# Kernel optimization log

Hardware: AMD Instinct MI355X
Metric: run time of the kernel (lower is better)

Reference implementation:

```python
import jax, jax.numpy as jnp
import numpy as np
from functools import partial

D_MODEL = 256
D_STATE = 16
DT_RANK = 16  # ceil(d_model/16)
LN_EPS = 1e-5


def setup_inputs() -> dict:
    key = jax.random.key(0)
    ks = jax.random.split(key, 8)
    B, L, d, N, r = 16, 2048, D_MODEL, D_STATE, DT_RANK
    x = jax.random.normal(ks[0], (B, L, d), dtype=jnp.float32)
    # LayerNorm params
    ln_w = jnp.ones((d,), jnp.float32)
    ln_b = jnp.zeros((d,), jnp.float32)
    # S6 params
    x_proj_w = jax.random.normal(ks[1], (d, r + 2 * N), jnp.float32) / np.sqrt(d)
    dt_proj_w = jax.random.normal(ks[2], (r, d), jnp.float32) / np.sqrt(r)
    dt_proj_b = jax.random.uniform(ks[3], (d,), jnp.float32, -4.0, -2.0)  # softplus -> small dt
    A_log = jnp.log(jnp.tile(jnp.arange(1, N + 1, dtype=jnp.float32), (d, 1)))  # (d, N)
    D_skip = jnp.ones((d,), jnp.float32)
    # GLU params
    glu_w = jax.random.normal(ks[4], (d, 2 * d), jnp.float32) / np.sqrt(d)
    glu_b = jnp.zeros((2 * d,), jnp.float32)
    return {"x": x, "ln_w": ln_w, "ln_b": ln_b, "x_proj_w": x_proj_w,
            "dt_proj_w": dt_proj_w, "dt_proj_b": dt_proj_b, "A_log": A_log,
            "D_skip": D_skip, "glu_w": glu_w, "glu_b": glu_b}


def _layernorm(x, w, b):
    mu = jnp.mean(x, -1, keepdims=True)
    var = jnp.mean(jnp.square(x - mu), -1, keepdims=True)
    return (x - mu) * jax.lax.rsqrt(var + LN_EPS) * w + b


def _s6(x, x_proj_w, dt_proj_w, dt_proj_b, A_log, D_skip):
    # x: (B, L, d) selective scan (S6)
    Bsz, L, d = x.shape
    N = A_log.shape[1]
    A = -jnp.exp(A_log)                       # (d, N)
    dbl = x @ x_proj_w                        # (B, L, r+2N)
    dt, Bm, Cm = jnp.split(dbl, [DT_RANK, DT_RANK + N], axis=-1)
    delta = jax.nn.softplus(dt @ dt_proj_w + dt_proj_b)  # (B, L, d)

    def step(h, inp):
        d_t, b_t, c_t, x_t = inp              # (B,d),(B,N),(B,N),(B,d)
        dA = jnp.exp(d_t[..., None] * A)      # (B, d, N)
        h = dA * h + (d_t * x_t)[..., None] * b_t[:, None, :]
        y = jnp.einsum('bdn,bn->bd', h, c_t)
        return h, y

    h0 = jnp.zeros((Bsz, d, N), x.dtype)
    xs = (jnp.swapaxes(delta, 0, 1), jnp.swapaxes(Bm, 0, 1),
          jnp.swapaxes(Cm, 0, 1), jnp.swapaxes(x, 0, 1))
    _, ys = jax.lax.scan(step, h0, xs)        # ys: (L, B, d)
    return jnp.swapaxes(ys, 0, 1) + x * D_skip


def _glu(x, w, b):
    d = x.shape[-1]
    out = x @ w + b
    return out[..., :d] * jax.nn.sigmoid(out[..., d:])


@jax.jit
def reference(x, ln_w, ln_b, x_proj_w, dt_proj_w, dt_proj_b, A_log, D_skip, glu_w, glu_b):
    skip = x
    h = _layernorm(x, ln_w, ln_b)
    h = _s6(h, x_proj_w, dt_proj_w, dt_proj_b, A_log, D_skip)
    h = jax.nn.gelu(h, approximate=False)     # dropout = identity (eval)
    h = _glu(h, glu_w, glu_b)
    return h + skip
```

## Files before the change

### kernel.cpp

```cpp
#include <hip/hip_runtime.h>
#include <hip/hip_bf16.h>

#define BB 16
#define LL 2048
#define DD 256
#define NN 16
#define RR 16
#define CHF 32
#define LCF 64
#define CHB 64
#define LCB 32

static __device__ __forceinline__ float bf2f(unsigned short u) {
    return __uint_as_float(((unsigned)u) << 16);
}
static __device__ __forceinline__ unsigned short f2bf(float f) {
    unsigned u = __float_as_uint(f);
    u += 0x7FFFu + ((u >> 16) & 1u);
    return (unsigned short)(u >> 16);
}

typedef __attribute__((ext_vector_type(8))) short bf16x8;
typedef __attribute__((ext_vector_type(4))) short bf16x4;
typedef __attribute__((ext_vector_type(4))) float f32x4;

static __device__ __forceinline__ void pow_tree(float E, float* e) {
    e[0] = E;
    e[1] = E * E;
    e[2] = e[1] * E;
    e[3] = e[1] * e[1];
    e[4] = e[3] * e[0];  e[5] = e[3] * e[1];  e[6] = e[3] * e[2];  e[7] = e[3] * e[3];
    e[8] = e[7] * e[0];  e[9] = e[7] * e[1];  e[10] = e[7] * e[2]; e[11] = e[7] * e[3];
    e[12] = e[7] * e[4]; e[13] = e[7] * e[5]; e[14] = e[7] * e[6]; e[15] = e[7] * e[7];
}

static __device__ __forceinline__ void gridBarrier(unsigned* bar, unsigned nblk) {
    __threadfence();
    __syncthreads();
    if (threadIdx.x == 0) {
        unsigned* cnt = bar;
        unsigned* gen = bar + 32;
        const unsigned gsnap = atomicAdd(gen, 0u);
        const unsigned arrived = atomicAdd(cnt, 1u) + 1u;
        if (arrived == nblk) {
            atomicExch(cnt, 0u);
            __threadfence();
            atomicAdd(gen, 1u);
        } else {
            while (atomicAdd(gen, 0u) == gsnap)
                __builtin_amdgcn_s_sleep(2);
        }
    }
    __syncthreads();
    __threadfence();
}

__global__ __launch_bounds__(256) void k_prep(
    const float* __restrict__ xw, const float* __restrict__ gw,
    unsigned short* __restrict__ Wxt, unsigned short* __restrict__ Wt)
{
    __shared__ unsigned short s[32][33];
    const int bid = blockIdx.x;
    const int t = threadIdx.x;
    if (bid < 16) {
        const int idx = bid * 256 + t;
        const int n  = idx >> 6;
        const int k0 = (idx & 63) * 4;
        #pragma unroll
        for (int i = 0; i < 4; ++i) {
            float v = (n < 48) ? xw[(size_t)(k0 + i) * 48 + n] : 0.f;
            Wxt[(size_t)n * DD + k0 + i] = f2bf(v);
        }
    } else {
        const int bb = bid - 16;
        const int bx = bb & 15, by = bb >> 4;
        const int r = t >> 5, cc = t & 31;
        #pragma unroll
        for (int i = 0; i < 4; ++i)
            s[r + 8*i][cc] = f2bf(gw[(size_t)(by*32 + r + 8*i)*512 + bx*32 + cc]);
        __syncthreads();
        #pragma unroll
        for (int i = 0; i < 4; ++i)
            Wt[(size_t)(bx*32 + r + 8*i)*256 + by*32 + cc] = s[cc][r + 8*i];
    }
}

template<bool FAST>
__device__ __forceinline__ void fused_scan1(
    const float (*sdt)[20], const unsigned short (*As)[264],
    const float (*sB)[17], const float* wj, float bia,
    const float* al, int t, float* h, float* dsum)
{
    #pragma unroll 4
    for (int l = 0; l < LCF; ++l) {
        float acc = bia;
        #pragma unroll
        for (int j = 0; j < 16; ++j)
            acc = fmaf(sdt[l][j], wj[j], acc);
        const float sp = (acc > 15.f) ? acc
            : 0.69314718f * log2f(1.f + exp2f(acc * 1.44269504f));
        const float dl = bf2f(f2bf(sp));
        const float xl = bf2f(As[l][t]);
        const float dx = dl * xl;
        *dsum += dl;
        float e[NN];
        if (FAST) pow_tree(exp2f(al[0]*dl), e);
        else {
            #pragma unroll
            for (int n = 0; n < NN; ++n) e[n] = exp2f(al[n]*dl);
        }
        #pragma unroll
        for (int n = 0; n < NN; ++n)
            h[n] = fmaf(e[n], h[n], dx * sB[l][n]);
    }
}

template<bool FAST>
__device__ __forceinline__ void fused_scan2(
    const float (*sdt)[20], const unsigned short (*As)[264],
    const float (*sB)[17], const float (*sC)[17],
    const float* wj, float bia, const float* al, int t,
    float* h, float dsk, size_t m0, unsigned short* __restrict__ g)
{
    #pragma unroll 4
    for (int l = 0; l < LCF; ++l) {
        float acc = bia;
        #pragma unroll
        for (int j = 0; j < 16; ++j)
            acc = fmaf(sdt[l][j], wj[j], acc);
        const float sp = (acc > 15.f) ? acc
            : 0.69314718f * log2f(1.f + exp2f(acc * 1.44269504f));
        const float dl = bf2f(f2bf(sp));
        const float xl = bf2f(As[l][t]);
        const float dx = dl * xl;
        float e[NN];
        if (FAST) pow_tree(exp2f(al[0]*dl), e);
        else {
            #pragma unroll
            for (int n = 0; n < NN; ++n) e[n] = exp2f(al[n]*dl);
        }
        float yb[4] = {0.f, 0.f, 0.f, 0.f};
        #pragma unroll
        for (int n = 0; n < NN; ++n) {
            h[n] = fmaf(e[n], h[n], dx * sB[l][n]);
            yb[n & 3] = fmaf(h[n], sC[l][n], yb[n & 3]);
        }
        const float vv = (yb[0]+yb[1]) + (yb[2]+yb[3]) + xl * dsk;
        const float u  = 0.7978845608f * (vv + 0.044715f*vv*vv*vv);
        const float t2 = exp2f(2.8853900818f * u);
        const float th = 1.f - 2.f/(t2 + 1.f);
        g[(m0 + l)*DD + t] = f2bf(0.5f * vv * (1.f + th));
    }
}

__global__ __launch_bounds__(256) void k_fused(
    const float* __restrict__ x,
    const float* __restrict__ ln_w,
    const float* __restrict__ ln_b,
    const unsigned short* __restrict__ Wxt,
    const float* __restrict__ dtw,
    const float* __restrict__ dtb,
    const float* __restrict__ A_log,
    const float* __restrict__ Dskip,
    float* __restrict__ S,
    float* __restrict__ Dsum,
    float* __restrict__ Hin,
    unsigned short* __restrict__ g,
    unsigned* __restrict__ bar)
{
    const int t = threadIdx.x;
    const int blk = blockIdx.x;
    const size_t m0 = (size_t)blk * LCF;

    __shared__ unsigned short As[LCF][264];
    __shared__ float sdt[LCF][20];
    __shared__ float sB[LCF][17];
    __shared__ float sC[LCF][17];
    __shared__ float slnw[256], slnb[256], sdtb[256];

    {
        const int tt = t & 63;
        if (t < 64)       *(float4*)&slnw[tt*4] = *(const float4*)&ln_w[tt*4];
        else if (t < 128) *(float4*)&slnb[tt*4] = *(const float4*)&ln_b[tt*4];
        else if (t < 192) *(float4*)&sdtb[tt*4] = *(const float4*)&dtb[tt*4];
    }

    float wj[16];
    #pragma unroll
    for (int j = 0; j < 16; ++j) wj[j] = dtw[j*DD + t];
    float al[NN];
    bool fast = true;
    #pragma unroll
    for (int n = 0; n < NN; ++n) {
        al[n] = -expf(A_log[t*NN + n]) * 1.44269504f;
        fast = fast && (fabsf(al[n] - (n+1)*al[0]) <= 1e-3f*fabsf(al[n]) + 1e-6f);
    }
    const float dsk = Dskip[t];
    __syncthreads();

    const int seg = t & 7;
    #pragma unroll
    for (int half = 0; half < 2; ++half) {
        const int row = (t >> 3) + 32*half;
        const size_t grow = m0 + row;
        float v[32];
        #pragma unroll
        for (int i = 0; i < 8; ++i)
            *(float4*)&v[i*4] = *(const float4*)(x + grow*DD + i*32 + seg*4);
        float s = 0.f, q = 0.f;
        #pragma unroll
        for (int i = 0; i < 32; ++i) { s += v[i]; q = fmaf(v[i], v[i], q); }
        #pragma unroll
        for (int o = 1; o < 8; o <<= 1) {
            s += __shfl_xor(s, o);
            q += __shfl_xor(q, o);
        }
        const float mu = s * (1.f/DD);
        const float rs = rsqrtf(q * (1.f/DD) - mu*mu + 1e-5f);
        #pragma unroll
        for (int i = 0; i < 8; ++i) {
            const int c = i*32 + seg*4;
            const float4 wv = *(const float4*)&slnw[c];
            const float4 bv = *(const float4*)&slnb[c];
            unsigned short o16[4];
            o16[0] = f2bf((v[i*4+0]-mu)*rs*wv.x + bv.x);
            o16[1] = f2bf((v[i*4+1]-mu)*rs*wv.y + bv.y);
            o16[2] = f2bf((v[i*4+2]-mu)*rs*wv.z + bv.z);
            o16[3] = f2bf((v[i*4+3]-mu)*rs*wv.w + bv.w);
            *(bf16x4*)&As[row][c] = *(bf16x4*)&o16[0];
        }
    }
    __syncthreads();

    {
        const int w = t >> 6, lane = t & 63;
        const int cl = lane & 15, rq = lane >> 4;
        const int mrow = w * 16;
        f32x4 aDt = {0.f,0.f,0.f,0.f}, aB = {0.f,0.f,0.f,0.f}, aC = {0.f,0.f,0.f,0.f};
        #pragma unroll
        for (int k0 = 0; k0 < 256; k0 += 32) {
            const bf16x8 a  = *(const bf16x8*)&As[mrow + cl][k0 + rq*8];
            const bf16x8 b0 = *(const bf16x8*)&Wxt[(size_t)(cl)*DD      + k0 + rq*8];
            const bf16x8 b1 = *(const bf16x8*)&Wxt[(size_t)(16+cl)*DD   + k0 + rq*8];
            const bf16x8 b2 = *(const bf16x8*)&Wxt[(size_t)(32+cl)*DD   + k0 + rq*8];
            aDt = __builtin_amdgcn_mfma_f32_16x16x32_bf16(a, b0, aDt, 0, 0, 0);
            aB  = __builtin_amdgcn_mfma_f32_16x16x32_bf16(a, b1, aB,  0, 0, 0);
            aC  = __builtin_amdgcn_mfma_f32_16x16x32_bf16(a, b2, aC,  0, 0, 0);
        }
        #pragma unroll
        for (int r = 0; r < 4; ++r) {
            const int rr = mrow + rq*4 + r;
            sdt[rr][cl] = aDt[r];
            sB[rr][cl]  = aB[r];
            sC[rr][cl]  = aC[r];
        }
    }
    __syncthreads();

    float h[NN];
    #pragma unroll
    for (int n = 0; n < NN; ++n) h[n] = 0.f;
    float dsum = 0.f;
    const float bia = sdtb[t];
    if (fast) fused_scan1<true >(sdt, As, sB, wj, bia, al, t, h, &dsum);
    else      fused_scan1<false>(sdt, As, sB, wj, bia, al, t, h, &dsum);
    {
        const size_t o = (size_t)blk * NN * DD + t;
        #pragma unroll
        for (int n = 0; n < NN; ++n) S[o + n*DD] = h[n];
        Dsum[(size_t)blk*DD + t] = dsum;
    }
    gridBarrier(bar, BB*CHF);

    if (blk < 256) {
        const int n2 = blk & 15, b2 = blk >> 4;
        const float al2 = -expf(A_log[t*NN + n2]) * 1.44269504f;
        float hh = 0.f;
        for (int c0 = 0; c0 < CHF; c0 += 16) {
            float ds16[16], s16[16];
            #pragma unroll
            for (int i = 0; i < 16; ++i) {
                const size_t bc = (size_t)b2*CHF + c0 + i;
                ds16[i] = Dsum[bc*DD + t];
                s16[i]  = S[(bc*NN + n2)*DD + t];
            }
            #pragma unroll
            for (int i = 0; i < 16; ++i) {
                const size_t bc = (size_t)b2*CHF + c0 + i;
                Hin[(bc*NN + n2)*DD + t] = hh;
                hh = fmaf(exp2f(al2 * ds16[i]), hh, s16[i]);
            }
        }
    }
    gridBarrier(bar, BB*CHF);

    {
        const size_t ob = (size_t)blk * NN * DD + t;
        #pragma unroll
        for (int n = 0; n < NN; ++n) h[n] = Hin[ob + n*DD];
    }
    if (fast) fused_scan2<true >(sdt, As, sB, sC, wj, bia, al, t, h, dsk, m0, g);
    else      fused_scan2<false>(sdt, As, sB, sC, wj, bia, al, t, h, dsk, m0, g);
}

template<bool FAST>
__device__ __forceinline__ void dt_scan1_fb(
    const float (*sdt)[20], const unsigned short (*As)[264],
    const float (*sB)[16], const float* wj, float bia,
    const float* al, int d, size_t m0,
    unsigned short* __restrict__ delta,
    float* h, float* dsum)
{
    #pragma unroll 4
    for (int l = 0; l < LCB; ++l) {
        float acc = bia;
        #pragma unroll
        for (int j = 0; j < 16; ++j)
            acc = fmaf(sdt[l][j], wj[j], acc);
        const float sp = (acc > 15.f) ? acc
            : 0.69314718f * log2f(1.f + exp2f(acc * 1.44269504f));
        const unsigned short dbits = f2bf(sp);
        delta[(m0 + l)*DD + d] = dbits;
        const float dl = bf2f(dbits);
        const float xl = bf2f(As[l][d]);
        const float dx = dl * xl;
        *dsum += dl;
        float e[NN];
        if (FAST) pow_tree(exp2f(al[0]*dl), e);
        else {
            #pragma unroll
            for (int n = 0; n < NN; ++n) e[n] = exp2f(al[n]*dl);
        }
        #pragma unroll
        for (int n = 0; n < NN; ++n)
            h[n] = fmaf(e[n], h[n], dx * sB[l][n]);
    }
}

__global__ __launch_bounds__(256) void k_ln_scan1(
    const float* __restrict__ x,
    const float* __restrict__ ln_w,
    const float* __restrict__ ln_b,
    const unsigned short* __restrict__ Wxt,
    const float* __restrict__ dtw,
    const float* __restrict__ dtb,
    const float* __restrict__ A_log,
    unsigned short* __restrict__ xln,
    unsigned short* __restrict__ delta,
    float* __restrict__ Bv,
    float* __restrict__ Cv,
    float* __restrict__ S,
    float* __restrict__ Dsum)
{
    const int t = threadIdx.x;
    const int blk = blockIdx.x;
    const size_t m0 = (size_t)blk * 32;
    const int row = t >> 3, seg = t & 7;
    const size_t grow = m0 + row;

    __shared__ unsigned short As[32][264];
    __shared__ float sdt[32][20];
    __shared__ float sB[32][16];
    __shared__ float slnw[256], slnb[256], sdtb[256];

    {
        const int tt = t & 63;
        if (t < 64)       *(float4*)&slnw[tt*4] = *(const float4*)&ln_w[tt*4];
        else if (t < 128) *(float4*)&slnb[tt*4] = *(const float4*)&ln_b[tt*4];
        else if (t < 192) *(float4*)&sdtb[tt*4] = *(const float4*)&dtb[tt*4];
    }
    float wj[16];
    #pragma unroll
    for (int j = 0; j < 16; ++j) wj[j] = dtw[j*DD + t];
    float al[NN];
    bool fast = true;
    #pragma unroll
    for (int n = 0; n < NN; ++n) {
        al[n] = -expf(A_log[t*NN + n]) * 1.44269504f;
        fast = fast && (fabsf(al[n] - (n+1)*al[0]) <= 1e-3f*fabsf(al[n]) + 1e-6f);
    }
    float v[32];
    #pragma unroll
    for (int i = 0; i < 8; ++i)
        *(float4*)&v[i*4] = *(const float4*)(x + grow*DD + i*32 + seg*4);
    float s = 0.f, q = 0.f;
    #pragma unroll
    for (int i = 0; i < 32; ++i) { s += v[i]; q = fmaf(v[i], v[i], q); }
    #pragma unroll
    for (int o = 1; o < 8; o <<= 1) {
        s += __shfl_xor(s, o);
        q += __shfl_xor(q, o);
    }
    const float mu = s * (1.f/DD);
    const float rs = rsqrtf(q * (1.f/DD) - mu*mu + 1e-5f);
    __syncthreads();
    #pragma unroll
    for (int i = 0; i < 8; ++i) {
        const int c = i*32 + seg*4;
        const float4 wv = *(const float4*)&slnw[c];
        const float4 bv = *(const float4*)&slnb[c];
        unsigned short o16[4];
        o16[0] = f2bf((v[i*4+0]-mu)*rs*wv.x + bv.x);
        o16[1] = f2bf((v[i*4+1]-mu)*rs*wv.y + bv.y);
        o16[2] = f2bf((v[i*4+2]-mu)*rs*wv.z + bv.z);
        o16[3] = f2bf((v[i*4+3]-mu)*rs*wv.w + bv.w);
        *(bf16x4*)&xln[grow*DD + c] = *(bf16x4*)&o16[0];
        *(bf16x4*)&As[row][c]       = *(bf16x4*)&o16[0];
    }
    __syncthreads();
    {
        const int w = t >> 6, lane = t & 63;
        const int cl = lane & 15, rq = lane >> 4;
        const int mh = (w & 1) * 16;
        const int nh = (w >> 1) * 32;
        f32x4 acc0 = {0.f,0.f,0.f,0.f}, acc1 = {0.f,0.f,0.f,0.f};
        #pragma unroll
        for (int k0 = 0; k0 < 256; k0 += 32) {
            const bf16x8 a  = *(const bf16x8*)&As[mh + cl][k0 + rq*8];
            const bf16x8 b0 = *(const bf16x8*)&Wxt[(size_t)(nh + cl)*DD + k0 + rq*8];
            acc0 = __builtin_amdgcn_mfma_f32_16x16x32_bf16(a, b0, acc0, 0, 0, 0);
            if (w < 2) {
                const bf16x8 b1 = *(const bf16x8*)&Wxt[(size_t)(nh + 16 + cl)*DD + k0 + rq*8];
                acc1 = __builtin_amdgcn_mfma_f32_16x16x32_bf16(a, b1, acc1, 0, 0, 0);
            }
        }
        if (w < 2) {
            #pragma unroll
            for (int r = 0; r < 4; ++r) {
                const int rr = mh + rq*4 + r;
                sdt[rr][cl] = acc0[r];
                sB[rr][cl]  = acc1[r];
                Bv[(m0 + rr)*NN + cl] = acc1[r];
            }
        } else {
            #pragma unroll
            for (int r = 0; r < 4; ++r)
                Cv[(m0 + mh + rq*4 + r)*NN + cl] = acc0[r];
        }
    }
    __syncthreads();
    float h[NN];
    #pragma unroll
    for (int n = 0; n < NN; ++n) h[n] = 0.f;
    float dsum = 0.f;
    const float bia = sdtb[t];
    if (fast) dt_scan1_fb<true >(sdt, As, sB, wj, bia, al, t, m0, delta, h, &dsum);
    else      dt_scan1_fb<false>(sdt, As, sB, wj, bia, al, t, m0, delta, h, &dsum);
    const size_t o = (size_t)blk * NN * DD + t;
    #pragma unroll
    for (int n = 0; n < NN; ++n) S[o + n*DD] = h[n];
    Dsum[(size_t)blk*DD + t] = dsum;
}

__global__ __launch_bounds__(256) void k_combine(
    const float* __restrict__ S, const float* __restrict__ Dsum,
    const float* __restrict__ A_log, float* __restrict__ Hin)
{
    const int bi = blockIdx.x;
    const int d = threadIdx.x;
    const int n = bi & 15;
    const int b = bi >> 4;
    const float al = -expf(A_log[d*NN + n]) * 1.44269504f;
    float h = 0.f;
    for (int c0 = 0; c0 < CHB; c0 += 8) {
        float ds8[8], s8[8];
        #pragma unroll
        for (int i = 0; i < 8; ++i) {
            const size_t blk = (size_t)b*CHB + c0 + i;
            ds8[i] = Dsum[blk*DD + d];
            s8[i]  = S[(blk*NN + n)*DD + d];
        }
        #pragma unroll
        for (int i = 0; i < 8; ++i) {
            const size_t blk = (size_t)b*CHB + c0 + i;
            Hin[(blk*NN + n)*DD + d] = h;
            h = fmaf(exp2f(al * ds8[i]), h, s8[i]);
        }
    }
}

template<bool FAST>
__device__ __forceinline__ void scan2_impl_fb(
    const unsigned short (*sD)[264], const unsigned short (*sX)[264],
    const float (*sB)[16], const float (*sC)[16],
    const float* al, int d, float* h, float dsk,
    size_t gout, unsigned short* __restrict__ g)
{
    #pragma unroll 4
    for (int l = 0; l < LCB; ++l) {
        const float dl = bf2f(sD[l][d]);
        const float xl = bf2f(sX[l][d]);
        const float dx = dl * xl;
        float e[NN];
        if (FAST) pow_tree(exp2f(al[0]*dl), e);
        else {
            #pragma unroll
            for (int n = 0; n < NN; ++n) e[n] = exp2f(al[n]*dl);
        }
        float yb[4] = {0.f, 0.f, 0.f, 0.f};
        #pragma unroll
        for (int n = 0; n < NN; ++n) {
            h[n] = fmaf(e[n], h[n], dx * sB[l][n]);
            yb[n & 3] = fmaf(h[n], sC[l][n], yb[n & 3]);
        }
        const float vv = (yb[0]+yb[1]) + (yb[2]+yb[3]) + xl * dsk;
        const float u  = 0.7978845608f * (vv + 0.044715f*vv*vv*vv);
        const float t2 = exp2f(2.8853900818f * u);
        const float th = 1.f - 2.f/(t2 + 1.f);
        g[gout + (size_t)l*DD] = f2bf(0.5f * vv * (1.f + th));
    }
}

__global__ __launch_bounds__(256) void k_scan2(
    const unsigned short* __restrict__ delta,
    const unsigned short* __restrict__ xln,
    const float* __restrict__ Bv,
    const float* __restrict__ Cv,
    const float* __restrict__ A_log,
    const float* __restrict__ Hin,
    const float* __restrict__ Dskip,
    unsigned short* __restrict__ g)
{
    const int blk = blockIdx.x;
    const int c = blk & (CHB-1);
    const int b = blk >> 6;
    const int d = threadIdx.x;
    const int l0 = c * LCB;
    __shared__ unsigned short sD[LCB][264];
    __shared__ unsigned short sX[LCB][264];
    __shared__ float sB[LCB][16], sC[LCB][16];
    {
        const int sr = d >> 3, sc = (d & 7) * 32;
        const size_t gbase = ((size_t)b*LL + l0 + sr)*DD + sc;
        #pragma unroll
        for (int i = 0; i < 4; ++i) {
            *(bf16x8*)&sD[sr][sc + i*8] = *(const bf16x8*)&delta[gbase + i*8];
            *(bf16x8*)&sX[sr][sc + i*8] = *(const bf16x8*)&xln  [gbase + i*8];
        }
        if (d < 128) {
            const int l = d >> 2, qq = (d & 3) * 4;
            *(float4*)&sB[l][qq] = *(const float4*)&Bv[((size_t)b*LL + l0 + l)*NN + qq];
        } else {
            const int dd = d - 128;
            const int l = dd >> 2, qq = (dd & 3) * 4;
            *(float4*)&sC[l][qq] = *(const float4*)&Cv[((size_t)b*LL + l0 + l)*NN + qq];
        }
    }
    float al[NN];
    bool fast = true;
    #pragma unroll
    for (int n = 0; n < NN; ++n) {
        al[n] = -expf(A_log[d*NN + n]) * 1.44269504f;
        fast = fast && (fabsf(al[n] - (n+1)*al[0]) <= 1e-3f*fabsf(al[n]) + 1e-6f);
    }
    float h[NN];
    const size_t ob = (size_t)blk * NN * DD + d;
    #pragma unroll
    for (int n = 0; n < NN; ++n) h[n] = Hin[ob + n*DD];
    const float dsk = Dskip[d];
    __syncthreads();
    const size_t gout = ((size_t)b*LL + l0)*DD + d;
    if (fast) scan2_impl_fb<true >(sD, sX, sB, sC, al, d, h, dsk, gout, g);
    else      scan2_impl_fb<false>(sD, sX, sB, sC, al, d, h, dsk, gout, g);
}

__global__ __launch_bounds__(256) void k_glu(
    const unsigned short* __restrict__ g,
    const unsigned short* __restrict__ Wt,
    const float* __restrict__ gb,
    const float* __restrict__ x,
    float* __restrict__ out)
{
    __shared__ unsigned short As[64][40];
    __shared__ unsigned short Bl[64][40];
    __shared__ unsigned short Bh[64][40];
    const int n0 = blockIdx.x * 64;
    const int m0 = blockIdx.y * 64;
    const int t = threadIdx.x;
    const int w = t >> 6, lane = t & 63;
    const int r = t >> 2, q = t & 3;
    const int cl = lane & 15, rq = lane >> 4;
    f32x4 accL[4], accH[4];
    const f32x4 zz = {0.f, 0.f, 0.f, 0.f};
    #pragma unroll
    for (int nf = 0; nf < 4; ++nf) { accL[nf] = zz; accH[nf] = zz; }

    for (int k0 = 0; k0 < 256; k0 += 32) {
        *(bf16x8*)(&As[r][q*8]) = *(const bf16x8*)(&g [(size_t)(m0+r)*DD + k0 + q*8]);
        *(bf16x8*)(&Bl[r][q*8]) = *(const bf16x8*)(&Wt[(size_t)(n0+r)*DD + k0 + q*8]);
        *(bf16x8*)(&Bh[r][q*8]) = *(const bf16x8*)(&Wt[(size_t)(n0+256+r)*DD + k0 + q*8]);
        __syncthreads();
        const bf16x8 a = *(const bf16x8*)(&As[w*16 + cl][rq*8]);
        #pragma unroll
        for (int nf = 0; nf < 4; ++nf) {
            const bf16x8 bl = *(const bf16x8*)(&Bl[nf*16 + cl][rq*8]);
            const bf16x8 bh = *(const bf16x8*)(&Bh[nf*16 + cl][rq*8]);
            accL[nf] = __builtin_amdgcn_mfma_f32_16x16x32_bf16(a, bl, accL[nf], 0, 0, 0);
            accH[nf] = __builtin_amdgcn_mfma_f32_16x16x32_bf16(a, bh, accH[nf], 0, 0, 0);
        }
        __syncthreads();
    }
    #pragma unroll
    for (int nf = 0; nf < 4; ++nf) {
        const int j = n0 + nf*16 + cl;
        const float bL = gb[j];
        const float bH = gb[j + 256];
        #pragma unroll
        for (int rr = 0; rr < 4; ++rr) {
            const int m = m0 + w*16 + rq*4 + rr;
            const float lo = accL[nf][rr] + bL;
            const float hi = accH[nf][rr] + bH;
            const float sg = 1.f / (1.f + exp2f(-1.44269504f * hi));
            out[(size_t)m*DD + j] = lo * sg + x[(size_t)m*DD + j];
        }
    }
}

extern "C" void kernel_launch(void* const* d_in, const int* in_sizes, int n_in,
                              void* d_out, int out_size, void* d_ws, size_t ws_size,
                              hipStream_t stream)
{
    const float* x    = (const float*)d_in[0];
    const float* ln_w = (const float*)d_in[1];
    const float* ln_b = (const float*)d_in[2];
    const float* xpw  = (const float*)d_in[3];
    const float* dtw  = (const float*)d_in[4];
    const float* dtb  = (const float*)d_in[5];
    const float* alog = (const float*)d_in[6];
    const float* dsk  = (const float*)d_in[7];
    const float* gw   = (const float*)d_in[8];
    const float* gb   = (const float*)d_in[9];
    float* out = (float*)d_out;

    char* ws = (char*)d_ws;
    size_t off = 0;
    auto alloc = [&](size_t bytes) {
        char* p = ws + off; off += (bytes + 255) & ~(size_t)255; return p;
    };
    unsigned*       bar    = (unsigned*)      alloc(256);
    unsigned short* xln    = (unsigned short*)alloc((size_t)BB*LL*DD*2);
    unsigned short* deltaG = (unsigned short*)alloc((size_t)BB*LL*DD*2);
    float*          Bvp    = (float*)         alloc((size_t)BB*LL*NN*4);
    float*          Cvp    = (float*)         alloc((size_t)BB*LL*NN*4);
    float*          S      = (float*)         alloc((size_t)BB*CHB*NN*DD*4);
    float*          Dsum   = (float*)         alloc((size_t)BB*CHB*DD*4);
    float*          Hin    = (float*)         alloc((size_t)BB*CHB*NN*DD*4);
    unsigned short* Wt     = (unsigned short*)alloc((size_t)512*256*2);
    unsigned short* Wxt    = (unsigned short*)alloc((size_t)64*256*2);
    unsigned short* g      = deltaG;

    k_prep<<<144, 256, 0, stream>>>(xpw, gw, Wxt, Wt);

    int occ = 0, ncu = 0, dev = 0;
    bool coop = false;
    if (hipGetDevice(&dev) == hipSuccess &&
        hipOccupancyMaxActiveBlocksPerMultiprocessor(&occ, k_fused, 256, 0) == hipSuccess &&
        hipDeviceGetAttribute(&ncu, hipDeviceAttributeMultiprocessorCount, dev) == hipSuccess)
        coop = (occ * ncu >= BB*CHF);

    if (coop) {
        hipMemsetAsync(bar, 0, 256, stream);
        k_fused<<<BB*CHF, 256, 0, stream>>>(x, ln_w, ln_b, Wxt, dtw, dtb, alog,
                                            dsk, S, Dsum, Hin, g, bar);
    } else {
        k_ln_scan1<<<BB*CHB, 256, 0, stream>>>(x, ln_w, ln_b, Wxt, dtw, dtb, alog,
                                               xln, deltaG, Bvp, Cvp, S, Dsum);
        k_combine<<<256, 256, 0, stream>>>(S, Dsum, alog, Hin);
        k_scan2<<<BB*CHB, 256, 0, stream>>>(deltaG, xln, Bvp, Cvp, alog, Hin, dsk, g);
    }

    k_glu<<<dim3(4, 512), 256, 0, stream>>>(g, Wt, gb, x, out);
}
```

Measured before the change: 110.1 us.

## Replace cooperative fused scan with three-kernel chunked scan using 128 chunks

Drops the single cooperative kernel that used software grid barriers and recomputed the dt projection in both scan passes. It goes back to three separate launches (LN + scan pass 1, combine, scan pass 2) with 128 chunks of 16 timesteps per batch instead of 32 chunks of 64. Pass 1 now stores delta, xln, B and C to global memory so pass 2 can reload them. The goal is more parallelism and no grid-barrier cost, paid for with extra global traffic, larger S/Hin buffers and a longer serial combine over 128 chunks.

Measured after the change: 118.4 us. +7.6%, slower.

```diff
diff --git a/kernel.cpp b/kernel.cpp
--- a/kernel.cpp
+++ b/kernel.cpp
@@ -1,13 +1,14 @@
 #include <hip/hip_runtime.h>
 #include <hip/hip_bf16.h>
+#include <cstring>
 
 #define BB 16
 #define LL 2048
 #define DD 256
 #define NN 16
 #define RR 16
-#define CHF 32
-#define LCF 64
+#define CH2 128
+#define LC2 16
 #define CHB 64
 #define LCB 32
 
@@ -34,27 +35,6 @@
     e[12] = e[7] * e[4]; e[13] = e[7] * e[5]; e[14] = e[7] * e[6]; e[15] = e[7] * e[7];
 }
 
-static __device__ __forceinline__ void gridBarrier(unsigned* bar, unsigned nblk) {
-    __threadfence();
-    __syncthreads();
-    if (threadIdx.x == 0) {
-        unsigned* cnt = bar;
-        unsigned* gen = bar + 32;
-        const unsigned gsnap = atomicAdd(gen, 0u);
-        const unsigned arrived = atomicAdd(cnt, 1u) + 1u;
-        if (arrived == nblk) {
-            atomicExch(cnt, 0u);
-            __threadfence();
-            atomicAdd(gen, 1u);
-        } else {
-            while (atomicAdd(gen, 0u) == gsnap)
-                __builtin_amdgcn_s_sleep(2);
-        }
-    }
-    __syncthreads();
-    __threadfence();
-}
-
 __global__ __launch_bounds__(256) void k_prep(
     const float* __restrict__ xw, const float* __restrict__ gw,
     unsigned short* __restrict__ Wxt, unsigned short* __restrict__ Wt)
@@ -85,22 +65,32 @@
     }
 }
 
+
 template<bool FAST>
-__device__ __forceinline__ void fused_scan1(
+__device__ __forceinline__ void dt_scan1_16(
     const float (*sdt)[20], const unsigned short (*As)[264],
     const float (*sB)[17], const float* wj, float bia,
-    const float* al, int t, float* h, float* dsum)
+    const float* al, int d, size_t m0,
+    unsigned short* __restrict__ delta,
+    float* h, float* dsum)
 {
     #pragma unroll 4
-    for (int l = 0; l < LCF; ++l) {
-        float acc = bia;
-        #pragma unroll
-        for (int j = 0; j < 16; ++j)
-            acc = fmaf(sdt[l][j], wj[j], acc);
+    for (int l = 0; l < LC2; ++l) {
+        float ab0 = bia, ab1 = 0.f, ab2 = 0.f, ab3 = 0.f;
+        #pragma unroll
+        for (int j = 0; j < 16; j += 4) {
+            ab0 = fmaf(sdt[l][j+0], wj[j+0], ab0);
+            ab1 = fmaf(sdt[l][j+1], wj[j+1], ab1);
+            ab2 = fmaf(sdt[l][j+2], wj[j+2], ab2);
+            ab3 = fmaf(sdt[l][j+3], wj[j+3], ab3);
+        }
+        const float acc = (ab0 + ab1) + (ab2 + ab3);
         const float sp = (acc > 15.f) ? acc
             : 0.69314718f * log2f(1.f + exp2f(acc * 1.44269504f));
-        const float dl = bf2f(f2bf(sp));
-        const float xl = bf2f(As[l][t]);
+        const unsigned short dbits = f2bf(sp);
+        delta[(m0 + l)*DD + d] = dbits;
+        const float dl = bf2f(dbits);
+        const float xl = bf2f(As[l][d]);
         const float dx = dl * xl;
         *dsum += dl;
         float e[NN];
@@ -115,45 +105,7 @@
     }
 }
 
-template<bool FAST>
-__device__ __forceinline__ void fused_scan2(
-    const float (*sdt)[20], const unsigned short (*As)[264],
-    const float (*sB)[17], const float (*sC)[17],
-    const float* wj, float bia, const float* al, int t,
-    float* h, float dsk, size_t m0, unsigned short* __restrict__ g)
-{
-    #pragma unroll 4
-    for (int l = 0; l < LCF; ++l) {
-        float acc = bia;
-        #pragma unroll
-        for (int j = 0; j < 16; ++j)
-            acc = fmaf(sdt[l][j], wj[j], acc);
-        const float sp = (acc > 15.f) ? acc
-            : 0.69314718f * log2f(1.f + exp2f(acc * 1.44269504f));
-        const float dl = bf2f(f2bf(sp));
-        const float xl = bf2f(As[l][t]);
-        const float dx = dl * xl;
-        float e[NN];
-        if (FAST) pow_tree(exp2f(al[0]*dl), e);
-        else {
-            #pragma unroll
-            for (int n = 0; n < NN; ++n) e[n] = exp2f(al[n]*dl);
-        }
-        float yb[4] = {0.f, 0.f, 0.f, 0.f};
-        #pragma unroll
-        for (int n = 0; n < NN; ++n) {
-            h[n] = fmaf(e[n], h[n], dx * sB[l][n]);
-            yb[n & 3] = fmaf(h[n], sC[l][n], yb[n & 3]);
-        }
-        const float vv = (yb[0]+yb[1]) + (yb[2]+yb[3]) + xl * dsk;
-        const float u  = 0.7978845608f * (vv + 0.044715f*vv*vv*vv);
-        const float t2 = exp2f(2.8853900818f * u);
-        const float th = 1.f - 2.f/(t2 + 1.f);
-        g[(m0 + l)*DD + t] = f2bf(0.5f * vv * (1.f + th));
-    }
-}
-
-__global__ __launch_bounds__(256) void k_fused(
+__global__ __launch_bounds__(256) void k_ln_scan1_16(
     const float* __restrict__ x,
     const float* __restrict__ ln_w,
     const float* __restrict__ ln_b,
@@ -161,21 +113,22 @@
     const float* __restrict__ dtw,
     const float* __restrict__ dtb,
     const float* __restrict__ A_log,
-    const float* __restrict__ Dskip,
+    unsigned short* __restrict__ xln,
+    unsigned short* __restrict__ delta,
+    float* __restrict__ Bv,
+    float* __restrict__ Cv,
     float* __restrict__ S,
-    float* __restrict__ Dsum,
-    float* __restrict__ Hin,
-    unsigned short* __restrict__ g,
-    unsigned* __restrict__ bar)
+    float* __restrict__ Dsum)
 {
     const int t = threadIdx.x;
     const int blk = blockIdx.x;
-    const size_t m0 = (size_t)blk * LCF;
-
-    __shared__ unsigned short As[LCF][264];
-    __shared__ float sdt[LCF][20];
-    __shared__ float sB[LCF][17];
-    __shared__ float sC[LCF][17];
+    const size_t m0 = (size_t)blk * LC2;
+    const int row = t >> 4, seg = t & 15;
+    const size_t grow = m0 + row;
+
+    __shared__ unsigned short As[LC2][264];
+    __shared__ float sdt[LC2][20];
+    __shared__ float sB[LC2][17];
     __shared__ float slnw[256], slnb[256], sdtb[256];
 
     {
@@ -184,7 +137,6 @@
         else if (t < 128) *(float4*)&slnb[tt*4] = *(const float4*)&ln_b[tt*4];
         else if (t < 192) *(float4*)&sdtb[tt*4] = *(const float4*)&dtb[tt*4];
     }
-
     float wj[16];
     #pragma unroll
     for (int j = 0; j < 16; ++j) wj[j] = dtw[j*DD + t];
@@ -195,64 +147,55 @@
         al[n] = -expf(A_log[t*NN + n]) * 1.44269504f;
         fast = fast && (fabsf(al[n] - (n+1)*al[0]) <= 1e-3f*fabsf(al[n]) + 1e-6f);
     }
-    const float dsk = Dskip[t];
-    __syncthreads();
-
-    const int seg = t & 7;
-    #pragma unroll
-    for (int half = 0; half < 2; ++half) {
-        const int row = (t >> 3) + 32*half;
-        const size_t grow = m0 + row;
-        float v[32];
-        #pragma unroll
-        for (int i = 0; i < 8; ++i)
-            *(float4*)&v[i*4] = *(const float4*)(x + grow*DD + i*32 + seg*4);
-        float s = 0.f, q = 0.f;
-        #pragma unroll
-        for (int i = 0; i < 32; ++i) { s += v[i]; q = fmaf(v[i], v[i], q); }
-        #pragma unroll
-        for (int o = 1; o < 8; o <<= 1) {
-            s += __shfl_xor(s, o);
-            q += __shfl_xor(q, o);
-        }
-        const float mu = s * (1.f/DD);
-        const float rs = rsqrtf(q * (1.f/DD) - mu*mu + 1e-5f);
-        #pragma unroll
-        for (int i = 0; i < 8; ++i) {
-            const int c = i*32 + seg*4;
-            const float4 wv = *(const float4*)&slnw[c];
-            const float4 bv = *(const float4*)&slnb[c];
-            unsigned short o16[4];
-            o16[0] = f2bf((v[i*4+0]-mu)*rs*wv.x + bv.x);
-            o16[1] = f2bf((v[i*4+1]-mu)*rs*wv.y + bv.y);
-            o16[2] = f2bf((v[i*4+2]-mu)*rs*wv.z + bv.z);
-            o16[3] = f2bf((v[i*4+3]-mu)*rs*wv.w + bv.w);
-            *(bf16x4*)&As[row][c] = *(bf16x4*)&o16[0];
-        }
+
+    float v[16];
+    #pragma unroll
+    for (int i = 0; i < 4; ++i)
+        *(float4*)&v[i*4] = *(const float4*)(x + grow*DD + i*64 + seg*4);
+    float s = 0.f, q = 0.f;
+    #pragma unroll
+    for (int i = 0; i < 16; ++i) { s += v[i]; q = fmaf(v[i], v[i], q); }
+    #pragma unroll
+    for (int o = 1; o < 16; o <<= 1) {
+        s += __shfl_xor(s, o);
+        q += __shfl_xor(q, o);
+    }
+    const float mu = s * (1.f/DD);
+    const float rs = rsqrtf(q * (1.f/DD) - mu*mu + 1e-5f);
+    __syncthreads();
+    #pragma unroll
+    for (int i = 0; i < 4; ++i) {
+        const int c = i*64 + seg*4;
+        const float4 wv = *(const float4*)&slnw[c];
+        const float4 bv = *(const float4*)&slnb[c];
+        unsigned short o16[4];
+        o16[0] = f2bf((v[i*4+0]-mu)*rs*wv.x + bv.x);
+        o16[1] = f2bf((v[i*4+1]-mu)*rs*wv.y + bv.y);
+        o16[2] = f2bf((v[i*4+2]-mu)*rs*wv.z + bv.z);
+        o16[3] = f2bf((v[i*4+3]-mu)*rs*wv.w + bv.w);
+        *(bf16x4*)&xln[grow*DD + c] = *(bf16x4*)&o16[0];
+        *(bf16x4*)&As[row][c]       = *(bf16x4*)&o16[0];
     }
     __syncthreads();
 
     {
         const int w = t >> 6, lane = t & 63;
         const int cl = lane & 15, rq = lane >> 4;
-        const int mrow = w * 16;
-        f32x4 aDt = {0.f,0.f,0.f,0.f}, aB = {0.f,0.f,0.f,0.f}, aC = {0.f,0.f,0.f,0.f};
-        #pragma unroll
-        for (int k0 = 0; k0 < 256; k0 += 32) {
-            const bf16x8 a  = *(const bf16x8*)&As[mrow + cl][k0 + rq*8];
-            const bf16x8 b0 = *(const bf16x8*)&Wxt[(size_t)(cl)*DD      + k0 + rq*8];
-            const bf16x8 b1 = *(const bf16x8*)&Wxt[(size_t)(16+cl)*DD   + k0 + rq*8];
-            const bf16x8 b2 = *(const bf16x8*)&Wxt[(size_t)(32+cl)*DD   + k0 + rq*8];
-            aDt = __builtin_amdgcn_mfma_f32_16x16x32_bf16(a, b0, aDt, 0, 0, 0);
-            aB  = __builtin_amdgcn_mfma_f32_16x16x32_bf16(a, b1, aB,  0, 0, 0);
-            aC  = __builtin_amdgcn_mfma_f32_16x16x32_bf16(a, b2, aC,  0, 0, 0);
-        }
-        #pragma unroll
-        for (int r = 0; r < 4; ++r) {
-            const int rr = mrow + rq*4 + r;
-            sdt[rr][cl] = aDt[r];
-            sB[rr][cl]  = aB[r];
-            sC[rr][cl]  = aC[r];
+        if (w < 3) {
+            f32x4 acc = {0.f,0.f,0.f,0.f};
+            #pragma unroll
+            for (int k0 = 0; k0 < 256; k0 += 32) {
+                const bf16x8 a = *(const bf16x8*)&As[cl][k0 + rq*8];
+                const bf16x8 b = *(const bf16x8*)&Wxt[(size_t)(w*16 + cl)*DD + k0 + rq*8];
+                acc = __builtin_amdgcn_mfma_f32_16x16x32_bf16(a, b, acc, 0, 0, 0);
+            }
+            #pragma unroll
+            for (int r = 0; r < 4; ++r) {
+                const int rr = rq*4 + r;
+                if (w == 0)      sdt[rr][cl] = acc[r];
+                else if (w == 1) { sB[rr][cl] = acc[r]; Bv[(m0 + rr)*NN + cl] = acc[r]; }
+                else             Cv[(m0 + rr)*NN + cl] = acc[r];
+            }
         }
     }
     __syncthreads();
@@ -262,45 +205,124 @@
     for (int n = 0; n < NN; ++n) h[n] = 0.f;
     float dsum = 0.f;
     const float bia = sdtb[t];
-    if (fast) fused_scan1<true >(sdt, As, sB, wj, bia, al, t, h, &dsum);
-    else      fused_scan1<false>(sdt, As, sB, wj, bia, al, t, h, &dsum);
+    if (fast) dt_scan1_16<true >(sdt, As, sB, wj, bia, al, t, m0, delta, h, &dsum);
+    else      dt_scan1_16<false>(sdt, As, sB, wj, bia, al, t, m0, delta, h, &dsum);
+    const size_t o = (size_t)blk * NN * DD + t;
+    #pragma unroll
+    for (int n = 0; n < NN; ++n) S[o + n*DD] = h[n];
+    Dsum[(size_t)blk*DD + t] = dsum;
+}
+
+__global__ __launch_bounds__(256) void k_combine_128(
+    const float* __restrict__ S, const float* __restrict__ Dsum,
+    const float* __restrict__ A_log, float* __restrict__ Hin)
+{
+    const int bi = blockIdx.x;
+    const int d = threadIdx.x;
+    const int n = bi & 15;
+    const int b = bi >> 4;
+    const float al = -expf(A_log[d*NN + n]) * 1.44269504f;
+    float h = 0.f;
+    for (int c0 = 0; c0 < CH2; c0 += 8) {
+        float ds8[8], s8[8];
+        #pragma unroll
+        for (int i = 0; i < 8; ++i) {
+            const size_t blk = (size_t)b*CH2 + c0 + i;
+            ds8[i] = Dsum[blk*DD + d];
+            s8[i]  = S[(blk*NN + n)*DD + d];
+        }
+        #pragma unroll
+        for (int i = 0; i < 8; ++i) {
+            const size_t blk = (size_t)b*CH2 + c0 + i;
+            Hin[(blk*NN + n)*DD + d] = h;
+            h = fmaf(exp2f(al * ds8[i]), h, s8[i]);
+        }
+    }
+}
+
+template<bool FAST>
+__device__ __forceinline__ void scan2_16(
+    const unsigned short (*sD)[264], const unsigned short (*sX)[264],
+    const float (*sB)[16], const float (*sC)[16],
+    const float* al, int d, float* h, float dsk,
+    size_t gout, unsigned short* __restrict__ g)
+{
+    #pragma unroll 4
+    for (int l = 0; l < LC2; ++l) {
+        const float dl = bf2f(sD[l][d]);
+        const float xl = bf2f(sX[l][d]);
+        const float dx = dl * xl;
+        float e[NN];
+        if (FAST) pow_tree(exp2f(al[0]*dl), e);
+        else {
+            #pragma unroll
+            for (int n = 0; n < NN; ++n) e[n] = exp2f(al[n]*dl);
+        }
+        float yb[4] = {0.f, 0.f, 0.f, 0.f};
+        #pragma unroll
+        for (int n = 0; n < NN; ++n) {
+            h[n] = fmaf(e[n], h[n], dx * sB[l][n]);
+            yb[n & 3] = fmaf(h[n], sC[l][n], yb[n & 3]);
+        }
+        const float vv = (yb[0]+yb[1]) + (yb[2]+yb[3]) + xl * dsk;
+        const float u  = 0.7978845608f * (vv + 0.044715f*vv*vv*vv);
+        const float t2 = exp2f(2.8853900818f * u);
+        const float th = 1.f - 2.f/(t2 + 1.f);
+        g[gout + (size_t)l*DD] = f2bf(0.5f * vv * (1.f + th));
+    }
+}
+
+__global__ __launch_bounds__(256) void k_scan2_16(
+    const unsigned short* __restrict__ delta,
+    const unsigned short* __restrict__ xln,
+    const float* __restrict__ Bv,
+    const float* __restrict__ Cv,
+    const float* __restrict__ A_log,
+    const float* __restrict__ Hin,
+    const float* __restrict__ Dskip,
+    unsigned short* __restrict__ g)
+{
+    const int blk = blockIdx.x;
+    const int c = blk & (CH2-1);
+    const int b = blk >> 7;
+    const int d = threadIdx.x;
+    const int l0 = c * LC2;
+    __shared__ unsigned short sD[LC2][264];
+    __shared__ unsigned short sX[LC2][264];
+    __shared__ float sB[LC2][16], sC[LC2][16];
     {
-        const size_t o = (size_t)blk * NN * DD + t;
-        #pragma unroll
-        for (int n = 0; n < NN; ++n) S[o + n*DD] = h[n];
-        Dsum[(size_t)blk*DD + t] = dsum;
-    }
-    gridBarrier(bar, BB*CHF);
-
-    if (blk < 256) {
-        const int n2 = blk & 15, b2 = blk >> 4;
-        const float al2 = -expf(A_log[t*NN + n2]) * 1.44269504f;
-        float hh = 0.f;
-        for (int c0 = 0; c0 < CHF; c0 += 16) {
-            float ds16[16], s16[16];
-            #pragma unroll
-            for (int i = 0; i < 16; ++i) {
-                const size_t bc = (size_t)b2*CHF + c0 + i;
-                ds16[i] = Dsum[bc*DD + t];
-                s16[i]  = S[(bc*NN + n2)*DD + t];
-            }
-            #pragma unroll
-            for (int i = 0; i < 16; ++i) {
-                const size_t bc = (size_t)b2*CHF + c0 + i;
-                Hin[(bc*NN + n2)*DD + t] = hh;
-                hh = fmaf(exp2f(al2 * ds16[i]), hh, s16[i]);
-            }
-        }
-    }
-    gridBarrier(bar, BB*CHF);
-
-    {
-        const size_t ob = (size_t)blk * NN * DD + t;
-        #pragma unroll
-        for (int n = 0; n < NN; ++n) h[n] = Hin[ob + n*DD];
-    }
-    if (fast) fused_scan2<true >(sdt, As, sB, sC, wj, bia, al, t, h, dsk, m0, g);
-    else      fused_scan2<false>(sdt, As, sB, sC, wj, bia, al, t, h, dsk, m0, g);
+        const int sr = d >> 4, scc = (d & 15) * 16;
+        const size_t gbase = ((size_t)b*LL + l0 + sr)*DD + scc;
+        #pragma unroll
+        for (int i = 0; i < 2; ++i) {
+            *(bf16x8*)&sD[sr][scc + i*8] = *(const bf16x8*)&delta[gbase + i*8];
+            *(bf16x8*)&sX[sr][scc + i*8] = *(const bf16x8*)&xln  [gbase + i*8];
+        }
+        if (d < 64) {
+            const int l = d >> 2, qq = (d & 3) * 4;
+            *(float4*)&sB[l][qq] = *(const float4*)&Bv[((size_t)b*LL + l0 + l)*NN + qq];
+        } else if (d < 128) {
+            const int dd = d - 64;
+            const int l = dd >> 2, qq = (dd & 3) * 4;
+            *(float4*)&sC[l][qq] = *(const float4*)&Cv[((size_t)b*LL + l0 + l)*NN + qq];
+        }
+    }
+    float al[NN];
+    bool fast = true;
+    #pragma unroll
+    for (int n = 0; n < NN; ++n) {
+        al[n] = -expf(A_log[d*NN + n]) * 1.44269504f;
+        fast = fast && (fabsf(al[n] - (n+1)*al[0]) <= 1e-3f*fabsf(al[n]) + 1e-6f);
+    }
+    float h[NN];
+    const size_t ob = (size_t)blk * NN * DD + d;
+    #pragma unroll
+    for (int n = 0; n < NN; ++n) h[n] = Hin[ob + n*DD];
+    const float dsk = Dskip[d];
+    __syncthreads();
+    const size_t gout = ((size_t)b*LL + l0)*DD + d;
+    if (fast) scan2_16<true >(sD, sX, sB, sC, al, d, h, dsk, gout, g);
+    else      scan2_16<false>(sD, sX, sB, sC, al, d, h, dsk, gout, g);
 }
 
 template<bool FAST>
@@ -637,32 +659,34 @@
     auto alloc = [&](size_t bytes) {
         char* p = ws + off; off += (bytes + 255) & ~(size_t)255; return p;
     };
-    unsigned*       bar    = (unsigned*)      alloc(256);
     unsigned short* xln    = (unsigned short*)alloc((size_t)BB*LL*DD*2);
     unsigned short* deltaG = (unsigned short*)alloc((size_t)BB*LL*DD*2);
     float*          Bvp    = (float*)         alloc((size_t)BB*LL*NN*4);
     float*          Cvp    = (float*)         alloc((size_t)BB*LL*NN*4);
-    float*          S      = (float*)         alloc((size_t)BB*CHB*NN*DD*4);
-    float*          Dsum   = (float*)         alloc((size_t)BB*CHB*DD*4);
-    float*          Hin    = (float*)         alloc((size_t)BB*CHB*NN*DD*4);
     unsigned short* Wt     = (unsigned short*)alloc((size_t)512*256*2);
     unsigned short* Wxt    = (unsigned short*)alloc((size_t)64*256*2);
     unsigned short* g      = deltaG;
 
+    size_t off128 = off;
+    auto alloc128 = [&](size_t bytes) {
+        char* p = ws + off128; off128 += (bytes + 255) & ~(size_t)255; return p;
+    };
+    float* S128    = (float*)alloc128((size_t)BB*CH2*NN*DD*4);
+    float* Dsum128 = (float*)alloc128((size_t)BB*CH2*DD*4);
+    float* Hin128  = (float*)alloc128((size_t)BB*CH2*NN*DD*4);
+    const bool use128 = (off128 <= ws_size);
+
     k_prep<<<144, 256, 0, stream>>>(xpw, gw, Wxt, Wt);
 
-    int occ = 0, ncu = 0, dev = 0;
-    bool coop = false;
-    if (hipGetDevice(&dev) == hipSuccess &&
-        hipOccupancyMaxActiveBlocksPerMultiprocessor(&occ, k_fused, 256, 0) == hipSuccess &&
-        hipDeviceGetAttribute(&ncu, hipDeviceAttributeMultiprocessorCount, dev) == hipSuccess)
-        coop = (occ * ncu >= BB*CHF);
-
-    if (coop) {
-        hipMemsetAsync(bar, 0, 256, stream);
-        k_fused<<<BB*CHF, 256, 0, stream>>>(x, ln_w, ln_b, Wxt, dtw, dtb, alog,
-                                            dsk, S, Dsum, Hin, g, bar);
+    if (use128) {
+        k_ln_scan1_16<<<BB*CH2, 256, 0, stream>>>(x, ln_w, ln_b, Wxt, dtw, dtb, alog,
+                                                  xln, deltaG, Bvp, Cvp, S128, Dsum128);
+        k_combine_128<<<256, 256, 0, stream>>>(S128, Dsum128, alog, Hin128);
+        k_scan2_16<<<BB*CH2, 256, 0, stream>>>(deltaG, xln, Bvp, Cvp, alog, Hin128, dsk, g);
     } else {
+        float* S    = (float*)alloc((size_t)BB*CHB*NN*DD*4);
+        float* Dsum = (float*)alloc((size_t)BB*CHB*DD*4);
+        float* Hin  = (float*)alloc((size_t)BB*CHB*NN*DD*4);
         k_ln_scan1<<<BB*CHB, 256, 0, stream>>>(x, ln_w, ln_b, Wxt, dtw, dtb, alog,
                                                xln, deltaG, Bvp, Cvp, S, Dsum);
         k_combine<<<256, 256, 0, stream>>>(S, Dsum, alog, Hin);
```
